# Kernel optimization log

Hardware: AMD Instinct MI355X
Metric: run time of the kernel (lower is better)

The kernel has to match this reference:

```python
import jax, jax.numpy as jnp
import numpy as np

DIM = 1024
NUM_HEADS = 16
HEAD_DIM = DIM // NUM_HEADS
SCALE = 1.0 / HEAD_DIM  # NOTE: module uses 1/head_dim, not 1/sqrt(head_dim)


def setup_inputs() -> dict:
    key = jax.random.key(0)
    ks = jax.random.split(key, 9)
    B, S = 2, 2048
    init = lambda k, shape: jax.random.normal(k, shape, dtype=jnp.float32) * 0.02
    return {
        "x": jax.random.normal(ks[0], (B, S, DIM), dtype=jnp.float32),
        "wq": init(ks[1], (DIM, DIM)), "bq": jnp.zeros((DIM,), jnp.float32),
        "wk": init(ks[2], (DIM, DIM)), "bk": jnp.zeros((DIM,), jnp.float32),
        "wv": init(ks[3], (DIM, DIM)), "bv": jnp.zeros((DIM,), jnp.float32),
        "wo": init(ks[4], (DIM, DIM)), "bo": jnp.zeros((DIM,), jnp.float32),
    }


def _attn(x, wq, bq, wk, bk, wv, bv, wo, bo):
    B, S, D = x.shape
    H, hd = NUM_HEADS, HEAD_DIM
    # projections; weights stored as (in, out) so y = x @ w + b
    q = (x @ wq + bq).reshape(B, S, H, hd).transpose(0, 2, 1, 3)  # [B,H,S,hd]
    k = (x @ wk + bk).reshape(B, S, H, hd).transpose(0, 2, 1, 3)
    v = (x @ wv + bv).reshape(B, S, H, hd).transpose(0, 2, 1, 3)
    scores = jnp.einsum("bhqd,bhkd->bhqk", q, k) * SCALE  # [B,H,S,S]
    # Module's mask: triu(ones, diagonal=0) kept -> attends to positions j >= i
    i = jnp.arange(S)[:, None]
    j = jnp.arange(S)[None, :]
    allowed = j >= i  # [S,S]
    scores = jnp.where(allowed[None, None], scores, -jnp.inf)
    probs = jax.nn.softmax(scores, axis=-1)
    # dropout is identity in eval/reference mode
    out = jnp.einsum("bhqk,bhkd->bhqd", probs, v)  # [B,H,S,hd]
    out = out.transpose(0, 2, 1, 3).reshape(B, S, D)
    return out @ wo + bo


def reference(x, wq, bq, wk, bk, wv, bv, wo, bo):
    return _attn(x, wq, bq, wk, bk, wv, bv, wo, bo)
```

## Files before the change

### kernel.cpp

```cpp
#include <hip/hip_runtime.h>
#include <hip/hip_bf16.h>


constexpr int NH    = 16;
constexpr int HD    = 64;
constexpr int BATCH = 2;
constexpr int SEQ   = 2048;
constexpr int DIMSZ = 1024;
constexpr float SCALE = 1.0f / 64.0f;
constexpr float QSCL = SCALE * 1.44269504088896f;

typedef __attribute__((ext_vector_type(8))) short short8;
typedef __attribute__((ext_vector_type(4))) short short4v;
typedef __attribute__((ext_vector_type(4))) float f32x4;
typedef __attribute__((ext_vector_type(4))) unsigned short ushort4v;

__device__ inline unsigned short f2bf(float f) {
    __hip_bfloat16 h = __float2bfloat16(f);
    unsigned short u;
    __builtin_memcpy(&u, &h, 2);
    return u;
}

__device__ __forceinline__ unsigned int cvt_pk_bf16(float lo, float hi) {
    unsigned int r;
    asm("v_cvt_pk_bf16_f32 %0, %1, %2" : "=v"(r) : "v"(lo), "v"(hi));
    return r;
}

__device__ __forceinline__ void gload_lds16(const void* g, void* l) {
    __builtin_amdgcn_global_load_lds(
        (const __attribute__((address_space(1))) unsigned int*)g,
        (__attribute__((address_space(3))) unsigned int*)l, 16, 0, 0);
}

__global__ __launch_bounds__(256) void cvt_x(const float* __restrict__ src,
                                             unsigned short* __restrict__ dst)
{
    const int i = blockIdx.x * 256 + threadIdx.x;
    const float4* s4 = reinterpret_cast<const float4*>(src);
    const float4 a = s4[(size_t)i * 2];
    const float4 b = s4[(size_t)i * 2 + 1];
    short8 o;
    o[0] = (short)f2bf(a.x); o[1] = (short)f2bf(a.y);
    o[2] = (short)f2bf(a.z); o[3] = (short)f2bf(a.w);
    o[4] = (short)f2bf(b.x); o[5] = (short)f2bf(b.y);
    o[6] = (short)f2bf(b.z); o[7] = (short)f2bf(b.w);
    *reinterpret_cast<short8*>(&dst[(size_t)i * 8]) = o;
}

__global__ __launch_bounds__(256) void cvt_w(const float* __restrict__ wq,
                                             const float* __restrict__ wk,
                                             const float* __restrict__ wv,
                                             const float* __restrict__ wo,
                                             unsigned short* __restrict__ wt)
{
    __shared__ float tile[64][65];
    const int t = threadIdx.x;
    const float* src = (blockIdx.z == 0) ? wq : (blockIdx.z == 1) ? wk
                     : (blockIdx.z == 2) ? wv : wo;
    const int n0 = blockIdx.x * 64, k0 = blockIdx.y * 64;

#pragma unroll
    for (int r = 0; r < 64; r += 16) {
        const int row = r + (t >> 4);
        const int c4 = (t & 15) * 4;
        const float4 v = *reinterpret_cast<const float4*>(
            &src[(size_t)(k0 + row) * DIMSZ + n0 + c4]);
        tile[row][c4 + 0] = v.x;
        tile[row][c4 + 1] = v.y;
        tile[row][c4 + 2] = v.z;
        tile[row][c4 + 3] = v.w;
    }
    __syncthreads();
#pragma unroll
    for (int rr = 0; rr < 2; ++rr) {
        const int n = rr * 32 + (t >> 3);
        const int kk0 = (t & 7) * 8;
        short8 pk;
#pragma unroll
        for (int e = 0; e < 8; ++e)
            pk[e] = (short)f2bf(tile[kk0 + e][n]);
        *reinterpret_cast<short8*>(
            &wt[((size_t)blockIdx.z * DIMSZ + n0 + n) * DIMSZ + k0 + kk0]) = pk;
    }
}

template <int EPI>
__global__ __launch_bounds__(256, 2) void mfma_gemm(
    const unsigned short* __restrict__ A, const unsigned short* __restrict__ Bt,
    const float* __restrict__ b0, const float* __restrict__ b1,
    const float* __restrict__ b2,
    unsigned short* __restrict__ q_o, unsigned short* __restrict__ k_o,
    unsigned short* __restrict__ vt_o, float* __restrict__ c_out)
{
    __shared__ unsigned short As[2][128 * 64];
    __shared__ unsigned short Bs[2][128 * 64];

    const int tid = threadIdx.x;
    const int lane = tid & 63;
    const int wv_ = tid >> 6;
    const int wr = wv_ >> 1, wc = wv_ & 1;
    const int c = lane & 15, g = lane >> 4;
    const int m0 = blockIdx.y * 128;
    const int nb0 = blockIdx.x * 128;
    const int wbase = (tid & 192) * 8;
    const int lrow = tid >> 3, ld0 = (tid & 7) * 8;

    f32x4 acc[4][4];
#pragma unroll
    for (int i = 0; i < 4; ++i)
#pragma unroll
        for (int j = 0; j < 4; ++j)
            acc[i][j] = (f32x4){0.f, 0.f, 0.f, 0.f};

    auto issue = [&](unsigned short* dA, unsigned short* dB, int k0) {
#pragma unroll
        for (int it = 0; it < 4; ++it) {
            const int row = it * 32 + lrow;
            gload_lds16(&A[(size_t)(m0 + row) * DIMSZ + k0 + ld0],
                        &dA[it * 2048 + wbase]);
            gload_lds16(&Bt[(size_t)(nb0 + row) * DIMSZ + k0 + ld0],
                        &dB[it * 2048 + wbase]);
        }
    };

    auto compute = [&](const unsigned short* Ac, const unsigned short* Bc) {
#pragma unroll
        for (int kk = 0; kk < 2; ++kk) {
            short8 af[4], bfr[4];
#pragma unroll
            for (int mi = 0; mi < 4; ++mi)
                af[mi] = *reinterpret_cast<const short8*>(
                    &Ac[(wr * 64 + mi * 16 + c) * 64 + kk * 32 + g * 8]);
#pragma unroll
            for (int ni = 0; ni < 4; ++ni)
                bfr[ni] = *reinterpret_cast<const short8*>(
                    &Bc[(wc * 64 + ni * 16 + c) * 64 + kk * 32 + g * 8]);
            __builtin_amdgcn_s_setprio(1);
#pragma unroll
            for (int mi = 0; mi < 4; ++mi)
#pragma unroll
                for (int ni = 0; ni < 4; ++ni)
                    acc[mi][ni] = __builtin_amdgcn_mfma_f32_16x16x32_bf16(
                        af[mi], bfr[ni], acc[mi][ni], 0, 0, 0);
            __builtin_amdgcn_s_setprio(0);
        }
    };

    issue(As[0], Bs[0], 0);
#pragma unroll 1
    for (int kt = 0; kt < DIMSZ / 64; kt += 2) {
        __syncthreads();
        if (kt + 1 < DIMSZ / 64) issue(As[1], Bs[1], (kt + 1) * 64);
        compute(As[0], Bs[0]);
        __syncthreads();
        if (kt + 2 < DIMSZ / 64) issue(As[0], Bs[0], (kt + 2) * 64);
        compute(As[1], Bs[1]);
    }

#pragma unroll
    for (int ni = 0; ni < 4; ++ni) {
        const int n_g = nb0 + wc * 64 + ni * 16 + c;
        if (EPI == 0) {
            const int which = n_g >> 10, nn = n_g & 1023;
            const int h = nn >> 6, d = nn & 63;
            const float bias = (which == 0 ? b0 : which == 1 ? b1 : b2)[nn];
#pragma unroll
            for (int mi = 0; mi < 4; ++mi) {
                const int m_g = m0 + wr * 64 + mi * 16 + g * 4;
                const int b = m_g >> 11, s = m_g & 2047;
                if (which == 0) {
#pragma unroll
                    for (int r = 0; r < 4; ++r)
                        q_o[((size_t)(b * NH + h) * SEQ + s + r) * HD + d] =
                            f2bf((acc[mi][ni][r] + bias) * QSCL);
                } else if (which == 1) {
#pragma unroll
                    for (int r = 0; r < 4; ++r)
                        k_o[((size_t)(b * NH + h) * SEQ + s + r) * HD + d] =
                            f2bf(acc[mi][ni][r] + bias);
                } else {
                    ushort4v pk;
#pragma unroll
                    for (int r = 0; r < 4; ++r)
                        pk[r] = f2bf(acc[mi][ni][r] + bias);
                    *reinterpret_cast<ushort4v*>(
                        &vt_o[((size_t)(b * NH + h) * HD + d) * SEQ + s]) = pk;
                }
            }
        } else {
            const float bias = b0[n_g];
#pragma unroll
            for (int mi = 0; mi < 4; ++mi) {
                const int m_g = m0 + wr * 64 + mi * 16 + g * 4;
#pragma unroll
                for (int r = 0; r < 4; ++r)
                    c_out[(size_t)(m_g + r) * DIMSZ + n_g] = acc[mi][ni][r] + bias;
            }
        }
    }
}

__device__ __forceinline__ void attn_tile(
    const short8 (&qa)[2], f32x4 (&accO)[4], float &m_run, float &l_run,
    const unsigned short* Ks, const unsigned short* Vts,
    const int c, const int g, const int w, const bool masked)
{
    constexpr int KS = 72;
    f32x4 st[4];
#pragma unroll
    for (int ni = 0; ni < 4; ++ni) st[ni] = (f32x4){0.f, 0.f, 0.f, 0.f};

    __builtin_amdgcn_s_setprio(1);
#pragma unroll
    for (int kk = 0; kk < 2; ++kk)
#pragma unroll
        for (int ni = 0; ni < 4; ++ni) {
            const short8 kf = *reinterpret_cast<const short8*>(
                &Ks[(ni * 16 + c) * KS + kk * 32 + g * 8]);
            st[ni] = __builtin_amdgcn_mfma_f32_16x16x32_bf16(
                kf, qa[kk], st[ni], 0, 0, 0);
        }
    __builtin_amdgcn_s_setprio(0);

    if (masked) {
#pragma unroll
        for (int ni = 0; ni < 4; ++ni)
#pragma unroll
            for (int r = 0; r < 4; ++r)
                if (ni * 16 + g * 4 + r < w * 16 + c) st[ni][r] = -1e30f;
    }

    float mx = -1e30f;
#pragma unroll
    for (int ni = 0; ni < 4; ++ni)
        mx = fmaxf(mx, fmaxf(fmaxf(st[ni][0], st[ni][1]),
                             fmaxf(st[ni][2], st[ni][3])));
    mx = fmaxf(mx, __shfl_xor(mx, 16));
    mx = fmaxf(mx, __shfl_xor(mx, 32));
    const float newm = fmaxf(m_run, mx);
    const float fac = exp2f(m_run - newm);
    float rs = 0.f;
#pragma unroll
    for (int ni = 0; ni < 4; ++ni)
#pragma unroll
        for (int r = 0; r < 4; ++r) {
            const float p = exp2f(st[ni][r] - newm);
            st[ni][r] = p;
            rs += p;
        }
    rs += __shfl_xor(rs, 16);
    rs += __shfl_xor(rs, 32);
    m_run = newm;
    l_run = l_run * fac + rs;

#pragma unroll
    for (int r = 0; r < 4; ++r) {
        const float fr = __int_as_float(__builtin_amdgcn_ds_bpermute(
            (g * 4 + r) * 4, __float_as_int(fac)));
#pragma unroll
        for (int ni = 0; ni < 4; ++ni) accO[ni][r] *= fr;
    }

    short8 pa[2];
#pragma unroll
    for (int kk = 0; kk < 2; ++kk) {
        union { unsigned int u[4]; short8 s; } pu;
        pu.u[0] = cvt_pk_bf16(st[2 * kk][0], st[2 * kk][1]);
        pu.u[1] = cvt_pk_bf16(st[2 * kk][2], st[2 * kk][3]);
        pu.u[2] = cvt_pk_bf16(st[2 * kk + 1][0], st[2 * kk + 1][1]);
        pu.u[3] = cvt_pk_bf16(st[2 * kk + 1][2], st[2 * kk + 1][3]);
        pa[kk] = pu.s;
    }

    __builtin_amdgcn_s_setprio(1);
#pragma unroll
    for (int kk = 0; kk < 2; ++kk)
#pragma unroll
        for (int ni = 0; ni < 4; ++ni) {
            union { short4v h[2]; short8 s; } vu;
            vu.h[0] = *reinterpret_cast<const short4v*>(
                &Vts[(ni * 16 + c) * KS + kk * 32 + g * 4]);
            vu.h[1] = *reinterpret_cast<const short4v*>(
                &Vts[(ni * 16 + c) * KS + kk * 32 + 16 + g * 4]);
            accO[ni] = __builtin_amdgcn_mfma_f32_16x16x32_bf16(
                pa[kk], vu.s, accO[ni], 0, 0, 0);
        }
    __builtin_amdgcn_s_setprio(0);
}

__global__ __launch_bounds__(256, 2) void flash_mfma(
    const unsigned short* __restrict__ q, const unsigned short* __restrict__ k,
    const unsigned short* __restrict__ vt, unsigned short* __restrict__ o)
{
    constexpr int KS = 72;
    __shared__ unsigned short Ks[64 * KS];
    __shared__ unsigned short Vts[64 * KS];

    const int tid = threadIdx.x, lane = tid & 63, w = tid >> 6;
    const int c = lane & 15, g = lane >> 4;
    const int qt1 = blockIdx.x;
    const int qt2 = 31 - qt1;
    const int h = blockIdx.y, b = blockIdx.z;
    const int head = b * NH + h;
    const unsigned short* kh = k + (size_t)head * SEQ * HD;
    const unsigned short* vth = vt + (size_t)head * HD * SEQ;

    short8 qa1[2], qa2[2];
    {
        const size_t qb1 = ((size_t)head * SEQ + qt1 * 64 + w * 16 + c) * HD;
        qa1[0] = *reinterpret_cast<const short8*>(&q[qb1 + g * 8]);
        qa1[1] = *reinterpret_cast<const short8*>(&q[qb1 + 32 + g * 8]);
        const size_t qb2 = ((size_t)head * SEQ + qt2 * 64 + w * 16 + c) * HD;
        qa2[0] = *reinterpret_cast<const short8*>(&q[qb2 + g * 8]);
        qa2[1] = *reinterpret_cast<const short8*>(&q[qb2 + 32 + g * 8]);
    }

    f32x4 acc1[4], acc2[4];
    float m1 = -1e30f, l1 = 0.f, m2 = -1e30f, l2 = 0.f;
#pragma unroll
    for (int i = 0; i < 4; ++i) {
        acc1[i] = (f32x4){0.f, 0.f, 0.f, 0.f};
        acc2[i] = (f32x4){0.f, 0.f, 0.f, 0.f};
    }

    short8 kreg[2], vreg[2];
    {
        const int j0 = qt1 * 64;
#pragma unroll
        for (int rr = 0; rr < 2; ++rr) {
            const int chunk = rr * 256 + tid;
            const int row = chunk >> 3, d0 = (chunk & 7) * 8;
            kreg[rr] = *reinterpret_cast<const short8*>(&kh[(size_t)(j0 + row) * HD + d0]);
            vreg[rr] = *reinterpret_cast<const short8*>(&vth[(size_t)row * SEQ + j0 + d0]);
        }
    }

    for (int jt = qt1; jt < SEQ / 64; ++jt) {
        __syncthreads();
#pragma unroll
        for (int rr = 0; rr < 2; ++rr) {
            const int chunk = rr * 256 + tid;
            const int row = chunk >> 3, d0 = (chunk & 7) * 8;
            *reinterpret_cast<short8*>(&Ks[row * KS + d0]) = kreg[rr];
            *reinterpret_cast<short8*>(&Vts[row * KS + d0]) = vreg[rr];
        }
        __syncthreads();
        if (jt + 1 < SEQ / 64) {
            const int j0 = (jt + 1) * 64;
#pragma unroll
            for (int rr = 0; rr < 2; ++rr) {
                const int chunk = rr * 256 + tid;
                const int row = chunk >> 3, d0 = (chunk & 7) * 8;
                kreg[rr] = *reinterpret_cast<const short8*>(&kh[(size_t)(j0 + row) * HD + d0]);
                vreg[rr] = *reinterpret_cast<const short8*>(&vth[(size_t)row * SEQ + j0 + d0]);
            }
        }

        attn_tile(qa1, acc1, m1, l1, Ks, Vts, c, g, w, jt == qt1);
        if (jt >= qt2)
            attn_tile(qa2, acc2, m2, l2, Ks, Vts, c, g, w, jt == qt2);
    }

#pragma unroll
    for (int r = 0; r < 4; ++r) {
        const float l1r = __int_as_float(__builtin_amdgcn_ds_bpermute(
            (g * 4 + r) * 4, __float_as_int(l1)));
        const float l2r = __int_as_float(__builtin_amdgcn_ds_bpermute(
            (g * 4 + r) * 4, __float_as_int(l2)));
        const float inv1 = 1.0f / l1r, inv2 = 1.0f / l2r;
#pragma unroll
        for (int ni = 0; ni < 4; ++ni) {
            const int d = ni * 16 + c;
            const int r1 = qt1 * 64 + w * 16 + g * 4 + r;
            o[((size_t)b * SEQ + r1) * DIMSZ + h * HD + d] =
                f2bf(acc1[ni][r] * inv1);
            const int r2 = qt2 * 64 + w * 16 + g * 4 + r;
            o[((size_t)b * SEQ + r2) * DIMSZ + h * HD + d] =
                f2bf(acc2[ni][r] * inv2);
        }
    }
}

extern "C" void kernel_launch(void* const* d_in, const int* in_sizes, int n_in,
                              void* d_out, int out_size, void* d_ws, size_t ws_size,
                              hipStream_t stream)
{
    const float* x  = (const float*)d_in[0];
    const float* wq = (const float*)d_in[1];
    const float* bq = (const float*)d_in[2];
    const float* wk = (const float*)d_in[3];
    const float* bk = (const float*)d_in[4];
    const float* wv = (const float*)d_in[5];
    const float* bv = (const float*)d_in[6];
    const float* wo = (const float*)d_in[7];
    const float* bo = (const float*)d_in[8];
    float* out = (float*)d_out;

    const size_t M4 = (size_t)4 * 1024 * 1024;
    unsigned short* p = (unsigned short*)d_ws;
    unsigned short* x_bf  = p;
    unsigned short* wt    = p + M4;
    unsigned short* q_bf  = p + 2 * M4;
    unsigned short* k_bf  = p + 3 * M4;
    unsigned short* vt_bf = p + 4 * M4;
    unsigned short* abf   = p + 5 * M4;

    cvt_x<<<2048, 256, 0, stream>>>(x, x_bf);
    cvt_w<<<dim3(16, 16, 4), 256, 0, stream>>>(wq, wk, wv, wo, wt);

    mfma_gemm<0><<<dim3(24, 32), 256, 0, stream>>>(
        x_bf, wt, bq, bk, bv, q_bf, k_bf, vt_bf, nullptr);

    flash_mfma<<<dim3(16, 16, 2), 256, 0, stream>>>(q_bf, k_bf, vt_bf, abf);

    mfma_gemm<1><<<dim3(8, 32), 256, 0, stream>>>(
        abf, wt + (size_t)3 * 1024 * 1024, bo, nullptr, nullptr,
        nullptr, nullptr, nullptr, out);
}
```

Before: 211.6 us.

## Stage QKV epilogue through LDS for coalesced stores; halve output GEMM M-tile

The QKV projection epilogue now writes bf16 results into shared memory first, then stores them to Q, K and transposed V with 16-byte contiguous writes. Before, each lane scattered 2-byte stores. Separately, the GEMM is templated on the M tile size, and the output projection uses 64-row tiles. That launches 512 blocks instead of 256, which should fill the CUs better. The cost is an extra LDS round trip and barrier in the epilogue, plus less data reuse per block in the output GEMM.

```diff
diff --git a/kernel.cpp b/kernel.cpp
--- a/kernel.cpp
+++ b/kernel.cpp
@@ -13,7 +13,6 @@
 typedef __attribute__((ext_vector_type(8))) short short8;
 typedef __attribute__((ext_vector_type(4))) short short4v;
 typedef __attribute__((ext_vector_type(4))) float f32x4;
-typedef __attribute__((ext_vector_type(4))) unsigned short ushort4v;
 
 __device__ inline unsigned short f2bf(float f) {
     __hip_bfloat16 h = __float2bfloat16(f);
@@ -86,7 +85,7 @@
     }
 }
 
-template <int EPI>
+template <int EPI, int BM>
 __global__ __launch_bounds__(256, 2) void mfma_gemm(
     const unsigned short* __restrict__ A, const unsigned short* __restrict__ Bt,
     const float* __restrict__ b0, const float* __restrict__ b1,
@@ -94,32 +93,40 @@
     unsigned short* __restrict__ q_o, unsigned short* __restrict__ k_o,
     unsigned short* __restrict__ vt_o, float* __restrict__ c_out)
 {
-    __shared__ unsigned short As[2][128 * 64];
-    __shared__ unsigned short Bs[2][128 * 64];
+    constexpr int MI = BM / 32;
+    __shared__ __align__(16) unsigned short smem[2 * BM * 64 + 2 * 128 * 64];
+    unsigned short* const A0 = smem;
+    unsigned short* const A1 = smem + BM * 64;
+    unsigned short* const B0 = smem + 2 * BM * 64;
+    unsigned short* const B1 = smem + 2 * BM * 64 + 128 * 64;
 
     const int tid = threadIdx.x;
     const int lane = tid & 63;
     const int wv_ = tid >> 6;
     const int wr = wv_ >> 1, wc = wv_ & 1;
     const int c = lane & 15, g = lane >> 4;
-    const int m0 = blockIdx.y * 128;
+    const int m0 = blockIdx.y * BM;
     const int nb0 = blockIdx.x * 128;
     const int wbase = (tid & 192) * 8;
     const int lrow = tid >> 3, ld0 = (tid & 7) * 8;
 
-    f32x4 acc[4][4];
-#pragma unroll
-    for (int i = 0; i < 4; ++i)
+    f32x4 acc[MI][4];
+#pragma unroll
+    for (int i = 0; i < MI; ++i)
 #pragma unroll
         for (int j = 0; j < 4; ++j)
             acc[i][j] = (f32x4){0.f, 0.f, 0.f, 0.f};
 
     auto issue = [&](unsigned short* dA, unsigned short* dB, int k0) {
 #pragma unroll
-        for (int it = 0; it < 4; ++it) {
+        for (int it = 0; it < BM / 32; ++it) {
             const int row = it * 32 + lrow;
             gload_lds16(&A[(size_t)(m0 + row) * DIMSZ + k0 + ld0],
                         &dA[it * 2048 + wbase]);
+        }
+#pragma unroll
+        for (int it = 0; it < 4; ++it) {
+            const int row = it * 32 + lrow;
             gload_lds16(&Bt[(size_t)(nb0 + row) * DIMSZ + k0 + ld0],
                         &dB[it * 2048 + wbase]);
         }
@@ -128,18 +135,18 @@
     auto compute = [&](const unsigned short* Ac, const unsigned short* Bc) {
 #pragma unroll
         for (int kk = 0; kk < 2; ++kk) {
-            short8 af[4], bfr[4];
-#pragma unroll
-            for (int mi = 0; mi < 4; ++mi)
+            short8 af[MI], bfr[4];
+#pragma unroll
+            for (int mi = 0; mi < MI; ++mi)
                 af[mi] = *reinterpret_cast<const short8*>(
-                    &Ac[(wr * 64 + mi * 16 + c) * 64 + kk * 32 + g * 8]);
+                    &Ac[(wr * (BM / 2) + mi * 16 + c) * 64 + kk * 32 + g * 8]);
 #pragma unroll
             for (int ni = 0; ni < 4; ++ni)
                 bfr[ni] = *reinterpret_cast<const short8*>(
                     &Bc[(wc * 64 + ni * 16 + c) * 64 + kk * 32 + g * 8]);
             __builtin_amdgcn_s_setprio(1);
 #pragma unroll
-            for (int mi = 0; mi < 4; ++mi)
+            for (int mi = 0; mi < MI; ++mi)
 #pragma unroll
                 for (int ni = 0; ni < 4; ++ni)
                     acc[mi][ni] = __builtin_amdgcn_mfma_f32_16x16x32_bf16(
@@ -148,52 +155,88 @@
         }
     };
 
-    issue(As[0], Bs[0], 0);
+    issue(A0, B0, 0);
 #pragma unroll 1
     for (int kt = 0; kt < DIMSZ / 64; kt += 2) {
         __syncthreads();
-        if (kt + 1 < DIMSZ / 64) issue(As[1], Bs[1], (kt + 1) * 64);
-        compute(As[0], Bs[0]);
+        if (kt + 1 < DIMSZ / 64) issue(A1, B1, (kt + 1) * 64);
+        compute(A0, B0);
         __syncthreads();
-        if (kt + 2 < DIMSZ / 64) issue(As[0], Bs[0], (kt + 2) * 64);
-        compute(As[1], Bs[1]);
-    }
-
-#pragma unroll
-    for (int ni = 0; ni < 4; ++ni) {
-        const int n_g = nb0 + wc * 64 + ni * 16 + c;
-        if (EPI == 0) {
-            const int which = n_g >> 10, nn = n_g & 1023;
-            const int h = nn >> 6, d = nn & 63;
-            const float bias = (which == 0 ? b0 : which == 1 ? b1 : b2)[nn];
-#pragma unroll
-            for (int mi = 0; mi < 4; ++mi) {
-                const int m_g = m0 + wr * 64 + mi * 16 + g * 4;
-                const int b = m_g >> 11, s = m_g & 2047;
-                if (which == 0) {
-#pragma unroll
-                    for (int r = 0; r < 4; ++r)
-                        q_o[((size_t)(b * NH + h) * SEQ + s + r) * HD + d] =
-                            f2bf((acc[mi][ni][r] + bias) * QSCL);
-                } else if (which == 1) {
-#pragma unroll
-                    for (int r = 0; r < 4; ++r)
-                        k_o[((size_t)(b * NH + h) * SEQ + s + r) * HD + d] =
-                            f2bf(acc[mi][ni][r] + bias);
-                } else {
-                    ushort4v pk;
-#pragma unroll
-                    for (int r = 0; r < 4; ++r)
-                        pk[r] = f2bf(acc[mi][ni][r] + bias);
-                    *reinterpret_cast<ushort4v*>(
-                        &vt_o[((size_t)(b * NH + h) * HD + d) * SEQ + s]) = pk;
+        if (kt + 2 < DIMSZ / 64) issue(A0, B0, (kt + 2) * 64);
+        compute(A1, B1);
+    }
+
+    if (EPI == 0) {
+        const int which = nb0 >> 10;
+        const int nn0 = nb0 & 1023;
+        const int h0 = nn0 >> 6;
+        const int b = m0 >> 11, s0 = m0 & 2047;
+        const float* bias_p = which == 0 ? b0 : which == 1 ? b1 : b2;
+        constexpr int LST = 136;
+        unsigned short* L = smem;
+
+        __syncthreads();
+        if (which == 2) {
+#pragma unroll
+            for (int mi = 0; mi < MI; ++mi)
+#pragma unroll
+                for (int ni = 0; ni < 4; ++ni) {
+                    const int n_l = wc * 64 + ni * 16 + c;
+                    const float bias = bias_p[nn0 + n_l];
+#pragma unroll
+                    for (int r = 0; r < 4; ++r) {
+                        const int s_l = wr * 64 + mi * 16 + g * 4 + r;
+                        L[n_l * LST + s_l] = f2bf(acc[mi][ni][r] + bias);
+                    }
                 }
+            __syncthreads();
+#pragma unroll
+            for (int p = 0; p < 8; ++p) {
+                const int idx = p * 256 + tid;
+                const int drow = idx >> 4;
+                const int so = (idx & 15) * 8;
+                const short8 vv = *reinterpret_cast<const short8*>(
+                    &L[drow * LST + so]);
+                const int hh = drow >> 6, d = drow & 63;
+                *reinterpret_cast<short8*>(
+                    &vt_o[((size_t)(b * NH + h0 + hh) * HD + d) * SEQ + s0 + so]) = vv;
             }
         } else {
+            unsigned short* dst = which == 0 ? q_o : k_o;
+            const float scl = which == 0 ? QSCL : 1.0f;
+#pragma unroll
+            for (int mi = 0; mi < MI; ++mi)
+#pragma unroll
+                for (int ni = 0; ni < 4; ++ni) {
+                    const int n_l = wc * 64 + ni * 16 + c;
+                    const float bias = bias_p[nn0 + n_l];
+#pragma unroll
+                    for (int r = 0; r < 4; ++r) {
+                        const int s_l = wr * 64 + mi * 16 + g * 4 + r;
+                        L[s_l * LST + n_l] = f2bf((acc[mi][ni][r] + bias) * scl);
+                    }
+                }
+            __syncthreads();
+#pragma unroll
+            for (int p = 0; p < 8; ++p) {
+                const int idx = p * 256 + tid;
+                const int hh = idx >> 10;
+                const int eo = (idx & 1023) * 8;
+                const int s_l = eo >> 6, d0 = eo & 63;
+                const short8 vv = *reinterpret_cast<const short8*>(
+                    &L[s_l * LST + hh * 64 + d0]);
+                *reinterpret_cast<short8*>(
+                    &dst[((size_t)(b * NH + h0 + hh) * SEQ + s0) * HD + eo]) = vv;
+            }
+        }
+    } else {
+#pragma unroll
+        for (int ni = 0; ni < 4; ++ni) {
+            const int n_g = nb0 + wc * 64 + ni * 16 + c;
             const float bias = b0[n_g];
 #pragma unroll
-            for (int mi = 0; mi < 4; ++mi) {
-                const int m_g = m0 + wr * 64 + mi * 16 + g * 4;
+            for (int mi = 0; mi < MI; ++mi) {
+                const int m_g = m0 + wr * (BM / 2) + mi * 16 + g * 4;
 #pragma unroll
                 for (int r = 0; r < 4; ++r)
                     c_out[(size_t)(m_g + r) * DIMSZ + n_g] = acc[mi][ni][r] + bias;
@@ -410,12 +453,12 @@
     cvt_x<<<2048, 256, 0, stream>>>(x, x_bf);
     cvt_w<<<dim3(16, 16, 4), 256, 0, stream>>>(wq, wk, wv, wo, wt);
 
-    mfma_gemm<0><<<dim3(24, 32), 256, 0, stream>>>(
+    mfma_gemm<0, 128><<<dim3(24, 32), 256, 0, stream>>>(
         x_bf, wt, bq, bk, bv, q_bf, k_bf, vt_bf, nullptr);
 
     flash_mfma<<<dim3(16, 16, 2), 256, 0, stream>>>(q_bf, k_bf, vt_bf, abf);
 
-    mfma_gemm<1><<<dim3(8, 32), 256, 0, stream>>>(
+    mfma_gemm<1, 64><<<dim3(8, 64), 256, 0, stream>>>(
         abf, wt + (size_t)3 * 1024 * 1024, bo, nullptr, nullptr,
         nullptr, nullptr, nullptr, out);
 }
```

Measured after the change: 200.3 us. 1.06x faster.
